# Kernel tuning notes

Hardware: AMD Instinct MI355X
Metric: run time of the kernel (lower is better)

The kernel has to match this reference:

```python
import jax, jax.numpy as jnp
import numpy as np

N = 16384          # batch
K = 4096           # num_neurons per LogicLayer
L = 4              # num_layers
IN0 = 4            # first layer in_dim (= 2*D from cat([x,-x]))
CLASSES = 2
TAU = 1.0


def setup_inputs() -> dict:
    key = jax.random.key(0)
    k1, k2, k3 = jax.random.split(key, 3)
    rng = np.random.default_rng(0)
    x = jax.random.normal(k1, (N, 2), dtype=jnp.float32)
    w0 = jax.random.normal(k2, (K, 16), dtype=jnp.float32)
    ws = jax.random.normal(k3, (L - 1, K, 16), dtype=jnp.float32)
    ia0 = jnp.asarray(rng.integers(0, IN0, size=(K,)), dtype=jnp.int32)
    ib0 = jnp.asarray(rng.integers(0, IN0, size=(K,)), dtype=jnp.int32)
    ia = jnp.asarray(rng.integers(0, K, size=(L - 1, K)), dtype=jnp.int32)
    ib = jnp.asarray(rng.integers(0, K, size=(L - 1, K)), dtype=jnp.int32)
    return dict(x=x, w0=w0, ws=ws, ia0=ia0, ib0=ib0, ia=ia, ib=ib)


def logic_layer(h, w, idx_a, idx_b):
    """Differentiable logic layer (difflogic, training mode).

    out = sum_i softmax(w)_i * op_i(a, b) over the 16 two-input boolean
    functions. All 16 ops are multilinear in (a, b), so the weighted sum
    collapses exactly to c0 + ca*a + cb*b + cab*a*b with per-neuron coeffs.
    """
    p = jax.nn.softmax(w, axis=-1)  # [k, 16]
    a = h[:, idx_a]                 # [N, k]
    b = h[:, idx_b]                 # [N, k]
    ca = p[:, 2] + p[:, 3] + p[:, 6] + p[:, 7] - p[:, 8] - p[:, 9] - p[:, 12] - p[:, 13]
    cb = p[:, 4] + p[:, 5] + p[:, 6] + p[:, 7] - p[:, 8] - p[:, 9] - p[:, 10] - p[:, 11]
    cab = (p[:, 1] - p[:, 2] - p[:, 4] - 2.0 * p[:, 6] - p[:, 7]
           + p[:, 8] + 2.0 * p[:, 9] + p[:, 11] + p[:, 13] - p[:, 14])
    c0 = p[:, 8] + p[:, 9] + p[:, 10] + p[:, 11] + p[:, 12] + p[:, 13] + p[:, 14] + p[:, 15]
    return c0 + ca * a + cb * b + cab * (a * b)


def _model(iv, w0, ws, ia0, ib0, ia, ib):
    h = logic_layer(iv, w0, ia0, ib0)
    for l in range(ws.shape[0]):  # small fixed layer loop
        h = logic_layer(h, ws[l], ia[l], ib[l])
    # GroupSum(class_count=2, tau=1.0)
    return h.reshape(h.shape[0], CLASSES, -1).sum(-1) / TAU


def reference(x, w0, ws, ia0, ib0, ia, ib):
    mx = jnp.concatenate([x, -x], axis=1)  # [N, 4]
    thresh_space = 0.5

    # ---- ti = 0: thresh = 0, flags all zero -> input_values = tx ----
    tx = (mx > 0.0).astype(jnp.float32)
    iv = tx
    rt0 = _model(iv, w0, ws, ia0, ib0, ia, ib)          # [N, 2]
    # flags[n,d,o] = 1 where input_values[n,d] != results[n,0,o]
    flags = (iv[:, :, None] != rt0[:, None, :]).astype(jnp.float32)  # [N, 4, 2]

    # ---- ti = 1 ----
    lastl = jnp.argmax(rt0, axis=1)                      # [N]
    wadj = jnp.where(lastl > 0, thresh_space, -thresh_space)
    thresh = wadj                                        # started from zeros
    tx = (mx > thresh[:, None]).astype(jnp.float32)
    # nested oi-loop writes tx wherever flags[n,d,oi]==0 for any oi
    upd = jnp.any(flags == 0.0, axis=2)                  # [N, 4]
    iv = jnp.where(upd, tx, iv)
    rt1 = _model(iv, w0, ws, ia0, ib0, ia, ib)           # [N, 2]
    return rt1
```

## Files before the change

### kernel.cpp

```cpp
#include <hip/hip_runtime.h>
#include <hip/hip_fp16.h>

#define KN 4096
#define NSAMP 16384

__global__ __launch_bounds__(256) void prep(
    const float* __restrict__ w0, const float* __restrict__ wsG,
    const int* __restrict__ ia0, const int* __restrict__ ib0,
    const int* __restrict__ ia, const int* __restrict__ ib,
    const float* __restrict__ x,
    uint4* __restrict__ desc, unsigned char* __restrict__ pats) {
    const int bid = blockIdx.x, tid = threadIdx.x;
    if (bid < 64) {
        int g = bid * 256 + tid;
        int layer = g >> 12, k = g & 4095;
        const float* wp = (layer == 0) ? w0 + (size_t)k * 16
                                       : wsG + ((size_t)(layer - 1) * KN + k) * 16;
        const float4* wr = (const float4*)wp;
        float4 v0 = wr[0], v1 = wr[1], v2 = wr[2], v3 = wr[3];
        float e0 = __expf(v0.x), e1 = __expf(v0.y), e2 = __expf(v0.z), e3 = __expf(v0.w);
        float e4 = __expf(v1.x), e5 = __expf(v1.y), e6 = __expf(v1.z), e7 = __expf(v1.w);
        float e8 = __expf(v2.x), e9 = __expf(v2.y), e10 = __expf(v2.z), e11 = __expf(v2.w);
        float e12 = __expf(v3.x), e13 = __expf(v3.y), e14 = __expf(v3.z), e15 = __expf(v3.w);
        float s = ((e0 + e1) + (e2 + e3)) + ((e4 + e5) + (e6 + e7))
                + ((e8 + e9) + (e10 + e11)) + ((e12 + e13) + (e14 + e15));
        float can  = ((e2 + e3) + (e6 + e7)) - ((e8 + e9) + (e12 + e13));
        float cbn  = ((e4 + e5) + (e6 + e7)) - ((e8 + e9) + (e10 + e11));
        float cabn = (e1 - e2) - (e4 + e7) - 2.0f * e6 + (e8 + e11) + 2.0f * e9
                   + (e13 - e14);
        float c0n  = ((e8 + e9) + (e10 + e11)) + ((e12 + e13) + (e14 + e15));
        float inv = 1.0f / s;
        int A = (layer == 0) ? ia0[k] : ia[(layer - 1) * KN + k];
        int B = (layer == 0) ? ib0[k] : ib[(layer - 1) * KN + k];
        __half2 p01 = __floats2half2_rn(c0n * inv, can * inv);
        __half2 p23 = __floats2half2_rn(cbn * inv, cabn * inv);
        uint4 d;
        d.x = *(unsigned*)&p01;
        d.y = *(unsigned*)&p23;
        d.z = (unsigned)A;
        d.w = (unsigned)B;
        desc[g] = d;
    } else {
        int n = (bid - 64) * 256 + tid;
        float2 xv = ((const float2*)x)[n];
        int p0 = (int)(xv.x > 0.0f) | ((int)(xv.y > 0.0f) << 1)
               | ((int)(-xv.x > 0.0f) << 2) | ((int)(-xv.y > 0.0f) << 3);
        pats[n] = (unsigned char)p0;
    }
}

__device__ __forceinline__ float neuron(uint4 d, float a, float b) {
    float2 c01 = __half22float2(*(__half2*)&d.x);
    float2 c23 = __half22float2(*(__half2*)&d.y);
    return c01.x + c01.y * a + c23.x * b + c23.y * (a * b);
}

__device__ void eval_desc(int pp, const uint4* __restrict__ desc,
                          float* h0, float* h1, float* red, int tid,
                          float& r0, float& r1) {
    #pragma unroll
    for (int i = 0; i < 4; ++i) {
        int k = tid + i * 1024;
        uint4 d = desc[k];
        float a = (float)((pp >> d.z) & 1), b = (float)((pp >> d.w) & 1);
        h0[k] = neuron(d, a, b);
    }
    __syncthreads();
    for (int l = 1; l <= 3; ++l) {
        const float* src = (l & 1) ? h0 : h1;
        float* dst = (l & 1) ? h1 : h0;
        #pragma unroll
        for (int i = 0; i < 4; ++i) {
            int k = tid + i * 1024;
            uint4 d = desc[l * KN + k];
            dst[k] = neuron(d, src[d.z], src[d.w]);
        }
        __syncthreads();
    }
    float s0 = h1[tid] + h1[tid + 1024];
    float s1 = h1[tid + 2048] + h1[tid + 3072];
    #pragma unroll
    for (int off = 32; off > 0; off >>= 1) {
        s0 += __shfl_down(s0, off, 64);
        s1 += __shfl_down(s1, off, 64);
    }
    int wid = tid >> 6, lane = tid & 63;
    if (lane == 0) { red[wid] = s0; red[16 + wid] = s1; }
    __syncthreads();
    if (tid == 0) {
        float t0 = 0.0f, t1 = 0.0f;
        #pragma unroll
        for (int wq = 0; wq < 16; ++wq) { t0 += red[wq]; t1 += red[16 + wq]; }
        red[32] = t0; red[33] = t1;
    }
    __syncthreads();
    r0 = red[32]; r1 = red[33];
    __syncthreads();
}

__global__ __launch_bounds__(1024) void table_scatter(
    const uint4* __restrict__ desc, const unsigned char* __restrict__ pats,
    const float* __restrict__ x, float* __restrict__ out) {
    __shared__ float h0[KN];
    __shared__ float h1[KN];
    __shared__ float red[34];
    __shared__ float tbl[32];
    const int pat = blockIdx.x;
    const int tid = threadIdx.x;

    uint4 dA[4], dB[4];
    #pragma unroll
    for (int i = 0; i < 4; ++i) {
        int k = tid + i * 1024;
        dA[i] = desc[k];
        dB[i] = desc[KN + k];
    }
    #pragma unroll
    for (int i = 0; i < 4; ++i) {
        int k = tid + i * 1024;
        float a = (float)((pat >> dA[i].z) & 1), b = (float)((pat >> dA[i].w) & 1);
        h0[k] = neuron(dA[i], a, b);
        dA[i] = desc[2 * KN + k];
    }
    __syncthreads();
    #pragma unroll
    for (int i = 0; i < 4; ++i) {
        int k = tid + i * 1024;
        h1[k] = neuron(dB[i], h0[dB[i].z], h0[dB[i].w]);
        dB[i] = desc[3 * KN + k];
    }
    __syncthreads();
    #pragma unroll
    for (int i = 0; i < 4; ++i) {
        int k = tid + i * 1024;
        h0[k] = neuron(dA[i], h1[dA[i].z], h1[dA[i].w]);
    }
    __syncthreads();
    float s0 = 0.0f, s1 = 0.0f;
    #pragma unroll
    for (int i = 0; i < 4; ++i) {
        float o = neuron(dB[i], h0[dB[i].z], h0[dB[i].w]);
        if (i < 2) s0 += o; else s1 += o;
    }
    #pragma unroll
    for (int off = 32; off > 0; off >>= 1) {
        s0 += __shfl_down(s0, off, 64);
        s1 += __shfl_down(s1, off, 64);
    }
    int wid = tid >> 6, lane = tid & 63;
    if (lane == 0) { red[wid] = s0; red[16 + wid] = s1; }
    __syncthreads();
    if (tid == 0) {
        float t0 = 0.0f, t1 = 0.0f;
        #pragma unroll
        for (int wq = 0; wq < 16; ++wq) { t0 += red[wq]; t1 += red[16 + wq]; }
        red[32] = t0; red[33] = t1;
    }
    __syncthreads();
    float r0 = red[32], r1 = red[33];

    bool slow = (r0 == 0.0f) || (r0 == 1.0f) || (r1 == 0.0f) || (r1 == 1.0f);
    if (!slow) {
        uint4 pv = ((const uint4*)pats)[tid];
        int base = tid * 16;
        unsigned wv[4] = { pv.x, pv.y, pv.z, pv.w };
        #pragma unroll
        for (int wq = 0; wq < 4; ++wq) {
            #pragma unroll
            for (int b = 0; b < 4; ++b) {
                if (((wv[wq] >> (8 * b)) & 0xffu) == (unsigned)pat) {
                    int n = base + wq * 4 + b;
                    ((float2*)out)[n] = make_float2(r0, r1);
                }
            }
        }
    } else {
        for (int pp = 0; pp < 16; ++pp) {
            float q0, q1;
            eval_desc(pp, desc, h0, h1, red, tid, q0, q1);
            if (tid == 0) { tbl[2 * pp] = q0; tbl[2 * pp + 1] = q1; }
        }
        __syncthreads();
        for (int n = tid; n < NSAMP; n += 1024) {
            if (pats[n] != (unsigned char)pat) continue;
            float2 xv = ((const float2*)x)[n];
            float mx[4] = { xv.x, xv.y, -xv.x, -xv.y };
            float ivf[4];
            int p0 = 0;
            #pragma unroll
            for (int i = 0; i < 4; ++i) {
                int b = mx[i] > 0.0f;
                ivf[i] = (float)b;
                p0 |= b << i;
            }
            float q0 = tbl[2 * p0], q1 = tbl[2 * p0 + 1];
            int lastl = (q1 > q0) ? 1 : 0;
            float thresh = lastl ? 0.5f : -0.5f;
            int p1 = 0;
            #pragma unroll
            for (int i = 0; i < 4; ++i) {
                bool upd = (ivf[i] == q0) || (ivf[i] == q1);
                int bit = upd ? (int)(mx[i] > thresh) : (int)ivf[i];
                p1 |= bit << i;
            }
            ((float2*)out)[n] = make_float2(tbl[2 * p1], tbl[2 * p1 + 1]);
        }
    }
}

extern "C" void kernel_launch(void* const* d_in, const int* in_sizes, int n_in,
                              void* d_out, int out_size, void* d_ws, size_t ws_size,
                              hipStream_t stream) {
    const float* x   = (const float*)d_in[0];
    const float* w0  = (const float*)d_in[1];
    const float* wsG = (const float*)d_in[2];
    const int* ia0   = (const int*)d_in[3];
    const int* ib0   = (const int*)d_in[4];
    const int* ia    = (const int*)d_in[5];
    const int* ib    = (const int*)d_in[6];

    uint4* desc         = (uint4*)d_ws;
    unsigned char* pats = (unsigned char*)d_ws + 4 * KN * 16;

    prep<<<128, 256, 0, stream>>>(w0, wsG, ia0, ib0, ia, ib, x, desc, pats);
    table_scatter<<<16, 1024, 0, stream>>>(desc, pats, x, (float*)d_out);
}
```

Measured before the change: 17.89 us.

## Precompute first-layer outputs per pattern and split descriptors into compact arrays

The prep kernel now evaluates layer 0 for all 16 input patterns and stores the results in h0all, so the table kernel loads h0 directly instead of computing it. Per-neuron descriptors are split into a 8-byte fp16 coefficient array and a packed 16-bit index pair, which cuts bytes loaded per neuron from 16 to 12. Prep launches more blocks and writes 256KB of extra data, which adds work to the first kernel in exchange for a shorter critical path in the 16-block second kernel.

```diff
diff --git a/kernel.cpp b/kernel.cpp
--- a/kernel.cpp
+++ b/kernel.cpp
@@ -3,45 +3,59 @@
 
 #define KN 4096
 #define NSAMP 16384
+
+
+__device__ __forceinline__ void softmax16(const float* __restrict__ wp,
+                                          float& c0, float& ca, float& cb, float& cab) {
+    const float4* wr = (const float4*)wp;
+    float4 v0 = wr[0], v1 = wr[1], v2 = wr[2], v3 = wr[3];
+    float e0 = __expf(v0.x), e1 = __expf(v0.y), e2 = __expf(v0.z), e3 = __expf(v0.w);
+    float e4 = __expf(v1.x), e5 = __expf(v1.y), e6 = __expf(v1.z), e7 = __expf(v1.w);
+    float e8 = __expf(v2.x), e9 = __expf(v2.y), e10 = __expf(v2.z), e11 = __expf(v2.w);
+    float e12 = __expf(v3.x), e13 = __expf(v3.y), e14 = __expf(v3.z), e15 = __expf(v3.w);
+    float s = ((e0 + e1) + (e2 + e3)) + ((e4 + e5) + (e6 + e7))
+            + ((e8 + e9) + (e10 + e11)) + ((e12 + e13) + (e14 + e15));
+    float can  = ((e2 + e3) + (e6 + e7)) - ((e8 + e9) + (e12 + e13));
+    float cbn  = ((e4 + e5) + (e6 + e7)) - ((e8 + e9) + (e10 + e11));
+    float cabn = (e1 - e2) - (e4 + e7) - 2.0f * e6 + (e8 + e11) + 2.0f * e9
+               + (e13 - e14);
+    float c0n  = ((e8 + e9) + (e10 + e11)) + ((e12 + e13) + (e14 + e15));
+    float inv = 1.0f / s;
+    c0 = c0n * inv; ca = can * inv; cb = cbn * inv; cab = cabn * inv;
+}
 
 __global__ __launch_bounds__(256) void prep(
     const float* __restrict__ w0, const float* __restrict__ wsG,
     const int* __restrict__ ia0, const int* __restrict__ ib0,
     const int* __restrict__ ia, const int* __restrict__ ib,
     const float* __restrict__ x,
-    uint4* __restrict__ desc, unsigned char* __restrict__ pats) {
+    uint2* __restrict__ cf16, unsigned* __restrict__ pidx,
+    float* __restrict__ h0all, unsigned char* __restrict__ pats) {
     const int bid = blockIdx.x, tid = threadIdx.x;
-    if (bid < 64) {
-        int g = bid * 256 + tid;
-        int layer = g >> 12, k = g & 4095;
-        const float* wp = (layer == 0) ? w0 + (size_t)k * 16
-                                       : wsG + ((size_t)(layer - 1) * KN + k) * 16;
-        const float4* wr = (const float4*)wp;
-        float4 v0 = wr[0], v1 = wr[1], v2 = wr[2], v3 = wr[3];
-        float e0 = __expf(v0.x), e1 = __expf(v0.y), e2 = __expf(v0.z), e3 = __expf(v0.w);
-        float e4 = __expf(v1.x), e5 = __expf(v1.y), e6 = __expf(v1.z), e7 = __expf(v1.w);
-        float e8 = __expf(v2.x), e9 = __expf(v2.y), e10 = __expf(v2.z), e11 = __expf(v2.w);
-        float e12 = __expf(v3.x), e13 = __expf(v3.y), e14 = __expf(v3.z), e15 = __expf(v3.w);
-        float s = ((e0 + e1) + (e2 + e3)) + ((e4 + e5) + (e6 + e7))
-                + ((e8 + e9) + (e10 + e11)) + ((e12 + e13) + (e14 + e15));
-        float can  = ((e2 + e3) + (e6 + e7)) - ((e8 + e9) + (e12 + e13));
-        float cbn  = ((e4 + e5) + (e6 + e7)) - ((e8 + e9) + (e10 + e11));
-        float cabn = (e1 - e2) - (e4 + e7) - 2.0f * e6 + (e8 + e11) + 2.0f * e9
-                   + (e13 - e14);
-        float c0n  = ((e8 + e9) + (e10 + e11)) + ((e12 + e13) + (e14 + e15));
-        float inv = 1.0f / s;
-        int A = (layer == 0) ? ia0[k] : ia[(layer - 1) * KN + k];
-        int B = (layer == 0) ? ib0[k] : ib[(layer - 1) * KN + k];
-        __half2 p01 = __floats2half2_rn(c0n * inv, can * inv);
-        __half2 p23 = __floats2half2_rn(cbn * inv, cabn * inv);
-        uint4 d;
-        d.x = *(unsigned*)&p01;
-        d.y = *(unsigned*)&p23;
-        d.z = (unsigned)A;
-        d.w = (unsigned)B;
-        desc[g] = d;
+    if (bid < 48) {
+        int g = KN + bid * 256 + tid;
+        int layer = g >> 12;
+        int k = g & 4095;
+        float c0, ca, cb, cab;
+        softmax16(wsG + ((size_t)(layer - 1) * KN + k) * 16, c0, ca, cb, cab);
+        __half2 p01 = __floats2half2_rn(c0, ca);
+        __half2 p23 = __floats2half2_rn(cb, cab);
+        uint2 c;
+        c.x = *(unsigned*)&p01;
+        c.y = *(unsigned*)&p23;
+        cf16[g] = c;
+        pidx[g] = (unsigned)ia[(layer - 1) * KN + k]
+                | ((unsigned)ib[(layer - 1) * KN + k] << 16);
+    } else if (bid < 304) {
+        int j = (bid - 48) * 256 + tid;
+        int pat = j >> 12, k = j & 4095;
+        float c0, ca, cb, cab;
+        softmax16(w0 + (size_t)k * 16, c0, ca, cb, cab);
+        float a = (float)((pat >> ia0[k]) & 1);
+        float b = (float)((pat >> ib0[k]) & 1);
+        h0all[j] = c0 + ca * a + cb * b + cab * (a * b);
     } else {
-        int n = (bid - 64) * 256 + tid;
+        int n = (bid - 304) * 256 + tid;
         float2 xv = ((const float2*)x)[n];
         int p0 = (int)(xv.x > 0.0f) | ((int)(xv.y > 0.0f) << 1)
                | ((int)(-xv.x > 0.0f) << 2) | ((int)(-xv.y > 0.0f) << 3);
@@ -49,21 +63,21 @@
     }
 }
 
-__device__ __forceinline__ float neuron(uint4 d, float a, float b) {
-    float2 c01 = __half22float2(*(__half2*)&d.x);
-    float2 c23 = __half22float2(*(__half2*)&d.y);
+__device__ __forceinline__ float neuron2(uint2 c, float a, float b) {
+    float2 c01 = __half22float2(*(__half2*)&c.x);
+    float2 c23 = __half22float2(*(__half2*)&c.y);
     return c01.x + c01.y * a + c23.x * b + c23.y * (a * b);
 }
 
-__device__ void eval_desc(int pp, const uint4* __restrict__ desc,
+__device__ void eval_full(int pp, const uint2* __restrict__ cf16,
+                          const unsigned* __restrict__ pidx,
+                          const float* __restrict__ h0all,
                           float* h0, float* h1, float* red, int tid,
                           float& r0, float& r1) {
     #pragma unroll
     for (int i = 0; i < 4; ++i) {
         int k = tid + i * 1024;
-        uint4 d = desc[k];
-        float a = (float)((pp >> d.z) & 1), b = (float)((pp >> d.w) & 1);
-        h0[k] = neuron(d, a, b);
+        h0[k] = h0all[pp * KN + k];
     }
     __syncthreads();
     for (int l = 1; l <= 3; ++l) {
@@ -72,8 +86,8 @@
         #pragma unroll
         for (int i = 0; i < 4; ++i) {
             int k = tid + i * 1024;
-            uint4 d = desc[l * KN + k];
-            dst[k] = neuron(d, src[d.z], src[d.w]);
+            unsigned xi = pidx[l * KN + k];
+            dst[k] = neuron2(cf16[l * KN + k], src[xi & 0xffff], src[xi >> 16]);
         }
         __syncthreads();
     }
@@ -99,7 +113,8 @@
 }
 
 __global__ __launch_bounds__(1024) void table_scatter(
-    const uint4* __restrict__ desc, const unsigned char* __restrict__ pats,
+    const uint2* __restrict__ cf16, const unsigned* __restrict__ pidx,
+    const float* __restrict__ h0all, const unsigned char* __restrict__ pats,
     const float* __restrict__ x, float* __restrict__ out) {
     __shared__ float h0[KN];
     __shared__ float h1[KN];
@@ -108,38 +123,39 @@
     const int pat = blockIdx.x;
     const int tid = threadIdx.x;
 
-    uint4 dA[4], dB[4];
-    #pragma unroll
-    for (int i = 0; i < 4; ++i) {
-        int k = tid + i * 1024;
-        dA[i] = desc[k];
-        dB[i] = desc[KN + k];
-    }
-    #pragma unroll
-    for (int i = 0; i < 4; ++i) {
-        int k = tid + i * 1024;
-        float a = (float)((pat >> dA[i].z) & 1), b = (float)((pat >> dA[i].w) & 1);
-        h0[k] = neuron(dA[i], a, b);
-        dA[i] = desc[2 * KN + k];
-    }
-    __syncthreads();
-    #pragma unroll
-    for (int i = 0; i < 4; ++i) {
-        int k = tid + i * 1024;
-        h1[k] = neuron(dB[i], h0[dB[i].z], h0[dB[i].w]);
-        dB[i] = desc[3 * KN + k];
-    }
-    __syncthreads();
-    #pragma unroll
-    for (int i = 0; i < 4; ++i) {
-        int k = tid + i * 1024;
-        h0[k] = neuron(dA[i], h1[dA[i].z], h1[dA[i].w]);
+    uint2 cB[4], cA[4];
+    unsigned xB[4], xA[4];
+    #pragma unroll
+    for (int i = 0; i < 4; ++i) {
+        int k = tid + i * 1024;
+        cB[i] = cf16[KN + k];      xB[i] = pidx[KN + k];
+        cA[i] = cf16[2 * KN + k];  xA[i] = pidx[2 * KN + k];
+    }
+    #pragma unroll
+    for (int i = 0; i < 4; ++i) {
+        int k = tid + i * 1024;
+        h0[k] = h0all[pat * KN + k];
+    }
+    __syncthreads();
+
+    #pragma unroll
+    for (int i = 0; i < 4; ++i) {
+        int k = tid + i * 1024;
+        h1[k] = neuron2(cB[i], h0[xB[i] & 0xffff], h0[xB[i] >> 16]);
+        cB[i] = cf16[3 * KN + k];
+        xB[i] = pidx[3 * KN + k];
+    }
+    __syncthreads();
+    #pragma unroll
+    for (int i = 0; i < 4; ++i) {
+        int k = tid + i * 1024;
+        h0[k] = neuron2(cA[i], h1[xA[i] & 0xffff], h1[xA[i] >> 16]);
     }
     __syncthreads();
     float s0 = 0.0f, s1 = 0.0f;
     #pragma unroll
     for (int i = 0; i < 4; ++i) {
-        float o = neuron(dB[i], h0[dB[i].z], h0[dB[i].w]);
+        float o = neuron2(cB[i], h0[xB[i] & 0xffff], h0[xB[i] >> 16]);
         if (i < 2) s0 += o; else s1 += o;
     }
     #pragma unroll
@@ -177,7 +193,7 @@
     } else {
         for (int pp = 0; pp < 16; ++pp) {
             float q0, q1;
-            eval_desc(pp, desc, h0, h1, red, tid, q0, q1);
+            eval_full(pp, cf16, pidx, h0all, h0, h1, red, tid, q0, q1);
             if (tid == 0) { tbl[2 * pp] = q0; tbl[2 * pp + 1] = q1; }
         }
         __syncthreads();
@@ -219,9 +235,13 @@
     const int* ia    = (const int*)d_in[5];
     const int* ib    = (const int*)d_in[6];
 
-    uint4* desc         = (uint4*)d_ws;
-    unsigned char* pats = (unsigned char*)d_ws + 4 * KN * 16;
-
-    prep<<<128, 256, 0, stream>>>(w0, wsG, ia0, ib0, ia, ib, x, desc, pats);
-    table_scatter<<<16, 1024, 0, stream>>>(desc, pats, x, (float*)d_out);
-}
+    uint2* cf16         = (uint2*)d_ws;
+    unsigned* pidx      = (unsigned*)((char*)d_ws + 131072);
+    float* h0all        = (float*)((char*)d_ws + 196608);
+    unsigned char* pats = (unsigned char*)d_ws + 458752;
+
+    prep<<<368, 256, 0, stream>>>(w0, wsG, ia0, ib0, ia, ib, x,
+                                  cf16, pidx, h0all, pats);
+    table_scatter<<<16, 1024, 0, stream>>>(cf16, pidx, h0all, pats, x,
+                                           (float*)d_out);
+}
```

New measurement: 17.32 us, median of 2. 3.2% less time.
